# Kernel optimization log

Measured on AMD Instinct MI355X. Metric: run time of the kernel, lower is better.

Reference implementation:

```python
import jax, jax.numpy as jnp
import numpy as np

N_HEAD = 12

def setup_inputs() -> dict:
    key = jax.random.key(0)
    ks = jax.random.split(key, 5)
    B, T, C = 2, 2048, 768
    s = 0.02
    return {
        "x": jax.random.normal(ks[0], (B, T, C), jnp.float32),
        "c_attn_w": jax.random.normal(ks[1], (C, 3 * C), jnp.float32) * s,
        "c_attn_b": jax.random.normal(ks[2], (3 * C,), jnp.float32) * s,
        "c_proj_w": jax.random.normal(ks[3], (C, C), jnp.float32) * s,
        "c_proj_b": jax.random.normal(ks[4], (C,), jnp.float32) * s,
    }

def reference(x, c_attn_w, c_attn_b, c_proj_w, c_proj_b):
    B, T, C = x.shape
    H = N_HEAD
    D = C // H
    qkv = x @ c_attn_w + c_attn_b              # [B,T,3C]
    q, k, v = jnp.split(qkv, 3, axis=-1)
    # [B,T,C] -> [B,H,T,D]
    q = q.reshape(B, T, H, D).transpose(0, 2, 1, 3)
    k = k.reshape(B, T, H, D).transpose(0, 2, 1, 3)
    v = v.reshape(B, T, H, D).transpose(0, 2, 1, 3)
    att = jnp.einsum('bhqd,bhkd->bhqk', q, k) * (1.0 / np.sqrt(D))
    causal = jnp.tril(jnp.ones((T, T), bool))  # [T,T]
    att = jnp.where(causal[None, None], att, jnp.float32(-jnp.inf))
    att = jax.nn.softmax(att, axis=-1)
    y = jnp.einsum('bhqk,bhkd->bhqd', att, v)  # [B,H,T,D]
    y = y.transpose(0, 2, 1, 3).reshape(B, T, C)
    return y @ c_proj_w + c_proj_b
```

## Files before the change

### kernel.cpp

```cpp
#include <hip/hip_runtime.h>
#include <hip/hip_bf16.h>


using half4   = __attribute__((ext_vector_type(4))) _Float16;
using half8   = __attribute__((ext_vector_type(8))) _Float16;
using floatx4 = __attribute__((ext_vector_type(4))) float;

#define T_SEQ 2048
#define NHEAD 12
#define HDIM 64
#define C3 2304
#define CDIM 768
#define BT 4096
#define BH 24

static __device__ inline _Float16 f2h(float f) { return (_Float16)f; }

__global__ __launch_bounds__(256)
void prologue(const float* __restrict__ x, const float* __restrict__ wa,
              const float* __restrict__ wp, _Float16* __restrict__ xb,
              _Float16* __restrict__ wTa, _Float16* __restrict__ wTp) {
    __shared__ float tile[32][33];
    int blk = blockIdx.x, tid = threadIdx.x;
    if (blk < 2304) {
        const float* w; _Float16* wT; int K, N, bx, by;
        if (blk < 1728) { w = wa; wT = wTa; K = CDIM; N = C3; bx = blk % 72; by = blk / 72; }
        else { int b2 = blk - 1728; w = wp; wT = wTp; K = CDIM; N = CDIM; bx = b2 % 24; by = b2 / 24; }
        int tx = tid & 31, ty = tid >> 5;
        #pragma unroll
        for (int j = 0; j < 32; j += 8) {
            int k = by * 32 + ty + j, n = bx * 32 + tx;
            tile[ty + j][tx] = w[(long)k * N + n];
        }
        __syncthreads();
        #pragma unroll
        for (int j = 0; j < 32; j += 8) {
            int nO = bx * 32 + ty + j, kO = by * 32 + tx;
            wT[(long)nO * K + kO] = f2h(tile[tx][ty + j]);
        }
    } else {
        int b2 = blk - 2304;
        long e0 = (long)b2 * 4096 + tid * 16;
        floatx4 f0 = *(const floatx4*)&x[e0];
        floatx4 f1 = *(const floatx4*)&x[e0 + 4];
        floatx4 f2 = *(const floatx4*)&x[e0 + 8];
        floatx4 f3 = *(const floatx4*)&x[e0 + 12];
        half8 h0, h1;
        #pragma unroll
        for (int j = 0; j < 4; ++j) {
            h0[j] = f2h(f0[j]); h0[4 + j] = f2h(f1[j]);
            h1[j] = f2h(f2[j]); h1[4 + j] = f2h(f3[j]);
        }
        *(half8*)&xb[e0] = h0;
        *(half8*)&xb[e0 + 8] = h1;
    }
}

__global__ __launch_bounds__(256)
void gemm_qkv(const _Float16* __restrict__ A, const _Float16* __restrict__ Bt,
              const float* __restrict__ bias,
              _Float16* __restrict__ Qb, _Float16* __restrict__ Kb,
              _Float16* __restrict__ Vt) {
    __shared__ __align__(16) _Float16 As[128 * 72];
    __shared__ __align__(16) _Float16 Bs[96 * 72];
    const int K = CDIM;
    int tid = threadIdx.x;
    int m0 = blockIdx.x * 128, n0 = blockIdx.y * 96;
    int w = tid >> 6, l = tid & 63;
    int wm = (w >> 1) * 64, wn = (w & 1) * 48;
    int lr = l & 15, lq = l >> 4;

    int rs = tid >> 3, cs = (tid & 7) * 8;

    floatx4 acc[4][3] = {};

    half8 Ar[4], Br[3];
    #pragma unroll
    for (int j = 0; j < 4; ++j)
        Ar[j] = *(const half8*)&A[(long)(m0 + j * 32 + rs) * K + cs];
    #pragma unroll
    for (int j = 0; j < 3; ++j)
        Br[j] = *(const half8*)&Bt[(long)(n0 + j * 32 + rs) * K + cs];

    for (int kb = 0; kb < K; kb += 64) {
        #pragma unroll
        for (int j = 0; j < 4; ++j)
            *(half8*)&As[(j * 32 + rs) * 72 + cs] = Ar[j];
        #pragma unroll
        for (int j = 0; j < 3; ++j)
            *(half8*)&Bs[(j * 32 + rs) * 72 + cs] = Br[j];
        __syncthreads();
        if (kb + 64 < K) {
            #pragma unroll
            for (int j = 0; j < 4; ++j)
                Ar[j] = *(const half8*)&A[(long)(m0 + j * 32 + rs) * K + kb + 64 + cs];
            #pragma unroll
            for (int j = 0; j < 3; ++j)
                Br[j] = *(const half8*)&Bt[(long)(n0 + j * 32 + rs) * K + kb + 64 + cs];
        }
        #pragma unroll
        for (int kh = 0; kh < 2; ++kh) {
            half8 af[4], bf[3];
            #pragma unroll
            for (int i = 0; i < 4; ++i)
                af[i] = *(const half8*)&As[(wm + i * 16 + lr) * 72 + kh * 32 + lq * 8];
            #pragma unroll
            for (int i = 0; i < 3; ++i)
                bf[i] = *(const half8*)&Bs[(wn + i * 16 + lr) * 72 + kh * 32 + lq * 8];
            #pragma unroll
            for (int mi = 0; mi < 4; ++mi)
                #pragma unroll
                for (int ni = 0; ni < 3; ++ni)
                    acc[mi][ni] = __builtin_amdgcn_mfma_f32_16x16x32_f16(af[mi], bf[ni], acc[mi][ni], 0, 0, 0);
        }
        __syncthreads();
    }

    int region = n0 / CDIM;
    if (region < 2) {
        _Float16* O = region ? Kb : Qb;
        int nc0 = n0 - region * CDIM + wn;
        #pragma unroll
        for (int mi = 0; mi < 4; ++mi)
            #pragma unroll
            for (int ni = 0; ni < 3; ++ni) {
                int col = nc0 + ni * 16 + lr;
                float bsc = bias[region * CDIM + col];
                #pragma unroll
                for (int r = 0; r < 4; ++r) {
                    int row = m0 + wm + mi * 16 + lq * 4 + r;
                    O[(long)row * CDIM + col] = f2h(acc[mi][ni][r] + bsc);
                }
            }
    } else {
        #pragma unroll
        for (int mi = 0; mi < 4; ++mi)
            #pragma unroll
            for (int ni = 0; ni < 3; ++ni) {
                int cv = n0 - 2 * CDIM + wn + ni * 16 + lr;
                float bsc = bias[2 * CDIM + cv];
                int h = cv >> 6, d = cv & 63;
                int t0 = m0 + wm + mi * 16 + lq * 4;
                int bb = t0 >> 11, t = t0 & 2047;
                half4 hv;
                #pragma unroll
                for (int r = 0; r < 4; ++r) hv[r] = f2h(acc[mi][ni][r] + bsc);
                *(half4*)&Vt[(((long)bb * NHEAD + h) * HDIM + d) * T_SEQ + t] = hv;
            }
    }
}

__global__ __launch_bounds__(256)
void gemm_proj(const _Float16* __restrict__ A, const _Float16* __restrict__ Bt,
               const float* __restrict__ bias, float* __restrict__ Cout) {
    __shared__ __align__(16) _Float16 As[64 * 72];
    __shared__ __align__(16) _Float16 Bs[96 * 72];
    const int K = CDIM, N = CDIM;
    int tid = threadIdx.x;
    int m0 = blockIdx.x * 64, n0 = blockIdx.y * 96;
    int w = tid >> 6, l = tid & 63;
    int wm = (w >> 1) * 32, wn = (w & 1) * 48;
    int lr = l & 15, lq = l >> 4;

    int rs = tid >> 3, cs = (tid & 7) * 8;

    floatx4 acc[2][3] = {};

    half8 Ar[2], Br[3];
    #pragma unroll
    for (int j = 0; j < 2; ++j)
        Ar[j] = *(const half8*)&A[(long)(m0 + j * 32 + rs) * K + cs];
    #pragma unroll
    for (int j = 0; j < 3; ++j)
        Br[j] = *(const half8*)&Bt[(long)(n0 + j * 32 + rs) * K + cs];

    for (int kb = 0; kb < K; kb += 64) {
        #pragma unroll
        for (int j = 0; j < 2; ++j)
            *(half8*)&As[(j * 32 + rs) * 72 + cs] = Ar[j];
        #pragma unroll
        for (int j = 0; j < 3; ++j)
            *(half8*)&Bs[(j * 32 + rs) * 72 + cs] = Br[j];
        __syncthreads();
        if (kb + 64 < K) {
            #pragma unroll
            for (int j = 0; j < 2; ++j)
                Ar[j] = *(const half8*)&A[(long)(m0 + j * 32 + rs) * K + kb + 64 + cs];
            #pragma unroll
            for (int j = 0; j < 3; ++j)
                Br[j] = *(const half8*)&Bt[(long)(n0 + j * 32 + rs) * K + kb + 64 + cs];
        }
        #pragma unroll
        for (int kh = 0; kh < 2; ++kh) {
            half8 af[2], bf[3];
            #pragma unroll
            for (int i = 0; i < 2; ++i)
                af[i] = *(const half8*)&As[(wm + i * 16 + lr) * 72 + kh * 32 + lq * 8];
            #pragma unroll
            for (int i = 0; i < 3; ++i)
                bf[i] = *(const half8*)&Bs[(wn + i * 16 + lr) * 72 + kh * 32 + lq * 8];
            #pragma unroll
            for (int mi = 0; mi < 2; ++mi)
                #pragma unroll
                for (int ni = 0; ni < 3; ++ni)
                    acc[mi][ni] = __builtin_amdgcn_mfma_f32_16x16x32_f16(af[mi], bf[ni], acc[mi][ni], 0, 0, 0);
        }
        __syncthreads();
    }
    #pragma unroll
    for (int mi = 0; mi < 2; ++mi)
        #pragma unroll
        for (int ni = 0; ni < 3; ++ni) {
            int col = n0 + wn + ni * 16 + lr;
            float b = bias[col];
            #pragma unroll
            for (int r = 0; r < 4; ++r) {
                int row = m0 + wm + mi * 16 + lq * 4 + r;
                Cout[(long)row * N + col] = acc[mi][ni][r] + b;
            }
        }
}

__global__ __launch_bounds__(128)
void attn_kernel(const _Float16* __restrict__ Qb, const _Float16* __restrict__ Kb,
                 const _Float16* __restrict__ Vt, _Float16* __restrict__ y) {
    __shared__ __align__(16) _Float16 Ks[128 * 72];
    __shared__ __align__(16) _Float16 Vs[64 * 136];
    __shared__ __align__(16) _Float16 Ps[2][32 * 136];
    int tid = threadIdx.x;
    int w = tid >> 6, l = tid & 63;
    int lr = l & 15, lq = l >> 4;
    int i = blockIdx.x;
    int round = i >> 8, c = i & 255;
    int r_ = (round == 0) ? c : (round == 1 ? 767 - c : 256 + c);
    int qb = 31 - r_ / 24;
    int bh = r_ % 24;
    int b = bh / NHEAD, h = bh % NHEAD;
    int q0w = qb * 64 + w * 32;

    const _Float16* Qp = Qb + (long)b * T_SEQ * CDIM + h * HDIM;
    const _Float16* Kg = Kb + (long)b * T_SEQ * CDIM + h * HDIM;
    const _Float16* Vg = Vt + (long)bh * HDIM * T_SEQ;

    int kr = tid >> 3, kc = (tid & 7) * 8;
    int vr = tid >> 4, vc = (tid & 15) * 8;

    const float qscale = 0.125f * 1.44269504f;
    half8 aq[2][2];
    #pragma unroll
    for (int s2 = 0; s2 < 2; ++s2)
        #pragma unroll
        for (int kk = 0; kk < 2; ++kk) {
            aq[s2][kk] = *(const half8*)&Qp[(long)(q0w + s2 * 16 + lr) * CDIM + kk * 32 + lq * 8];
            #pragma unroll
            for (int j = 0; j < 8; ++j) aq[s2][kk][j] = f2h((float)aq[s2][kk][j] * qscale);
        }

    int nk = (qb + 2) >> 1;

    half8 Kr[8], Vr[8];
    #pragma unroll
    for (int j = 0; j < 8; ++j) {
        Kr[j] = *(const half8*)&Kg[(long)(j * 16 + kr) * CDIM + kc];
        Vr[j] = *(const half8*)&Vg[(long)(j * 8 + vr) * T_SEQ + vc];
    }

    float psum[2] = {0.f, 0.f};
    floatx4 acc[4][2] = {};
    int qrow0 = q0w + lr, qrow1 = q0w + 16 + lr;

    for (int kt = 0; kt < nk; ++kt) {
        int kbase = kt * 128;
        #pragma unroll
        for (int j = 0; j < 8; ++j) {
            *(half8*)&Ks[(j * 16 + kr) * 72 + kc] = Kr[j];
            *(half8*)&Vs[(j * 8 + vr) * 136 + vc] = Vr[j];
        }
        __syncthreads();
        if (kt + 1 < nk) {
            int nb = kbase + 128;
            #pragma unroll
            for (int j = 0; j < 8; ++j) {
                Kr[j] = *(const half8*)&Kg[(long)(nb + j * 16 + kr) * CDIM + kc];
                Vr[j] = *(const half8*)&Vg[(long)(j * 8 + vr) * T_SEQ + nb + vc];
            }
        }

        floatx4 sacc[8][2];
        #pragma unroll
        for (int s = 0; s < 8; ++s)
            #pragma unroll
            for (int s2 = 0; s2 < 2; ++s2) sacc[s][s2] = floatx4{0.f, 0.f, 0.f, 0.f};
        #pragma unroll
        for (int s = 0; s < 8; ++s) {
            #pragma unroll
            for (int kh = 0; kh < 2; ++kh) {
                half8 bk = *(const half8*)&Ks[(s * 16 + lr) * 72 + kh * 32 + lq * 8];
                sacc[s][0] = __builtin_amdgcn_mfma_f32_16x16x32_f16(bk, aq[0][kh], sacc[s][0], 0, 0, 0);
                sacc[s][1] = __builtin_amdgcn_mfma_f32_16x16x32_f16(bk, aq[1][kh], sacc[s][1], 0, 0, 0);
            }
        }

        if (kt == nk - 1) {
            #pragma unroll
            for (int s = 0; s < 8; ++s) {
                half4 hv0, hv1;
                #pragma unroll
                for (int r = 0; r < 4; ++r) {
                    int key = kbase + s * 16 + lq * 4 + r;
                    float p0 = (key > qrow0) ? 0.f : __builtin_amdgcn_exp2f(sacc[s][0][r]);
                    float p1 = (key > qrow1) ? 0.f : __builtin_amdgcn_exp2f(sacc[s][1][r]);
                    psum[0] += p0; psum[1] += p1;
                    hv0[r] = f2h(p0); hv1[r] = f2h(p1);
                }
                *(half4*)&Ps[w][(lr) * 136 + s * 16 + lq * 4] = hv0;
                *(half4*)&Ps[w][(16 + lr) * 136 + s * 16 + lq * 4] = hv1;
            }
        } else {
            #pragma unroll
            for (int s = 0; s < 8; ++s) {
                half4 hv0, hv1;
                #pragma unroll
                for (int r = 0; r < 4; ++r) {
                    float p0 = __builtin_amdgcn_exp2f(sacc[s][0][r]);
                    float p1 = __builtin_amdgcn_exp2f(sacc[s][1][r]);
                    psum[0] += p0; psum[1] += p1;
                    hv0[r] = f2h(p0); hv1[r] = f2h(p1);
                }
                *(half4*)&Ps[w][(lr) * 136 + s * 16 + lq * 4] = hv0;
                *(half4*)&Ps[w][(16 + lr) * 136 + s * 16 + lq * 4] = hv1;
            }
        }

        half8 ap[2][4];
        #pragma unroll
        for (int s2 = 0; s2 < 2; ++s2)
            #pragma unroll
            for (int kk = 0; kk < 4; ++kk)
                ap[s2][kk] = *(const half8*)&Ps[w][(s2 * 16 + lr) * 136 + kk * 32 + lq * 8];
        #pragma unroll
        for (int n = 0; n < 4; ++n) {
            #pragma unroll
            for (int kk = 0; kk < 4; ++kk) {
                half8 bv = *(const half8*)&Vs[(n * 16 + lr) * 136 + kk * 32 + lq * 8];
                acc[n][0] = __builtin_amdgcn_mfma_f32_16x16x32_f16(ap[0][kk], bv, acc[n][0], 0, 0, 0);
                acc[n][1] = __builtin_amdgcn_mfma_f32_16x16x32_f16(ap[1][kk], bv, acc[n][1], 0, 0, 0);
            }
        }
        __syncthreads();
    }

    #pragma unroll
    for (int s2 = 0; s2 < 2; ++s2) {
        float L = psum[s2];
        L += __shfl_xor(L, 16, 64);
        L += __shfl_xor(L, 32, 64);
        float Lr[4];
        #pragma unroll
        for (int r = 0; r < 4; ++r) Lr[r] = __shfl(L, lq * 4 + r, 64);
        #pragma unroll
        for (int n = 0; n < 4; ++n)
            #pragma unroll
            for (int r = 0; r < 4; ++r) {
                int row = q0w + s2 * 16 + lq * 4 + r;
                float v = acc[n][s2][r] / Lr[r];
                y[((long)(b * T_SEQ) + row) * CDIM + h * HDIM + n * 16 + lr] = f2h(v);
            }
    }
}

extern "C" void kernel_launch(void* const* d_in, const int* in_sizes, int n_in,
                              void* d_out, int out_size, void* d_ws, size_t ws_size,
                              hipStream_t stream) {
    const float* x      = (const float*)d_in[0];
    const float* w_attn = (const float*)d_in[1];
    const float* b_attn = (const float*)d_in[2];
    const float* w_proj = (const float*)d_in[3];
    const float* b_proj = (const float*)d_in[4];
    float* out = (float*)d_out;

    char* ws = (char*)d_ws;
    _Float16* xb  = (_Float16*)(ws);
    _Float16* wTa = (_Float16*)(ws + 6291456);
    _Float16* wTp = (_Float16*)(ws + 9830400);
    _Float16* Qb  = (_Float16*)(ws + 11010048);
    _Float16* Kb  = (_Float16*)(ws + 17301504);
    _Float16* Vt  = (_Float16*)(ws + 23592960);
    _Float16* yb  = (_Float16*)(ws + 29884416);

    prologue<<<3072, 256, 0, stream>>>(x, w_attn, w_proj, xb, wTa, wTp);

    gemm_qkv<<<dim3(BT / 128, C3 / 96), 256, 0, stream>>>(xb, wTa, b_attn, Qb, Kb, Vt);

    attn_kernel<<<BH * (T_SEQ / 64), 128, 0, stream>>>(Qb, Kb, Vt, yb);

    gemm_proj<<<dim3(BT / 64, CDIM / 96), 256, 0, stream>>>(yb, wTp, b_proj, out);
}
```

Before: 141.8 us.

## Fuse x fp16 conversion into QKV GEMM and split attention keys across four waves

The QKV GEMM now loads the fp32 input directly and converts it to fp16 while staging into shared memory, so the prologue no longer converts x and the xb buffer is no longer written and then read back. The attention kernel moves from 128 to 256 threads: each 64-query block is handled by four waves, two of which take the first half of every 128-key tile and two the second half, and their partial outputs and row sums are combined through shared memory at the end. This gives each block more waves and smaller per-wave register tiles to hide latency. The cost is an extra LDS reduction and barrier, plus twice as many fp32 bytes read for the GEMM A operand, which each N-tile block fetches again.

```diff
diff --git a/kernel.cpp b/kernel.cpp
--- a/kernel.cpp
+++ b/kernel.cpp
@@ -17,47 +17,29 @@
 static __device__ inline _Float16 f2h(float f) { return (_Float16)f; }
 
 __global__ __launch_bounds__(256)
-void prologue(const float* __restrict__ x, const float* __restrict__ wa,
-              const float* __restrict__ wp, _Float16* __restrict__ xb,
+void prologue(const float* __restrict__ wa, const float* __restrict__ wp,
               _Float16* __restrict__ wTa, _Float16* __restrict__ wTp) {
     __shared__ float tile[32][33];
     int blk = blockIdx.x, tid = threadIdx.x;
-    if (blk < 2304) {
-        const float* w; _Float16* wT; int K, N, bx, by;
-        if (blk < 1728) { w = wa; wT = wTa; K = CDIM; N = C3; bx = blk % 72; by = blk / 72; }
-        else { int b2 = blk - 1728; w = wp; wT = wTp; K = CDIM; N = CDIM; bx = b2 % 24; by = b2 / 24; }
-        int tx = tid & 31, ty = tid >> 5;
-        #pragma unroll
-        for (int j = 0; j < 32; j += 8) {
-            int k = by * 32 + ty + j, n = bx * 32 + tx;
-            tile[ty + j][tx] = w[(long)k * N + n];
-        }
-        __syncthreads();
-        #pragma unroll
-        for (int j = 0; j < 32; j += 8) {
-            int nO = bx * 32 + ty + j, kO = by * 32 + tx;
-            wT[(long)nO * K + kO] = f2h(tile[tx][ty + j]);
-        }
-    } else {
-        int b2 = blk - 2304;
-        long e0 = (long)b2 * 4096 + tid * 16;
-        floatx4 f0 = *(const floatx4*)&x[e0];
-        floatx4 f1 = *(const floatx4*)&x[e0 + 4];
-        floatx4 f2 = *(const floatx4*)&x[e0 + 8];
-        floatx4 f3 = *(const floatx4*)&x[e0 + 12];
-        half8 h0, h1;
-        #pragma unroll
-        for (int j = 0; j < 4; ++j) {
-            h0[j] = f2h(f0[j]); h0[4 + j] = f2h(f1[j]);
-            h1[j] = f2h(f2[j]); h1[4 + j] = f2h(f3[j]);
-        }
-        *(half8*)&xb[e0] = h0;
-        *(half8*)&xb[e0 + 8] = h1;
+    const float* w; _Float16* wT; int K, N, bx, by;
+    if (blk < 1728) { w = wa; wT = wTa; K = CDIM; N = C3; bx = blk % 72; by = blk / 72; }
+    else { int b2 = blk - 1728; w = wp; wT = wTp; K = CDIM; N = CDIM; bx = b2 % 24; by = b2 / 24; }
+    int tx = tid & 31, ty = tid >> 5;
+    #pragma unroll
+    for (int j = 0; j < 32; j += 8) {
+        int k = by * 32 + ty + j, n = bx * 32 + tx;
+        tile[ty + j][tx] = w[(long)k * N + n];
+    }
+    __syncthreads();
+    #pragma unroll
+    for (int j = 0; j < 32; j += 8) {
+        int nO = bx * 32 + ty + j, kO = by * 32 + tx;
+        wT[(long)nO * K + kO] = f2h(tile[tx][ty + j]);
     }
 }
 
 __global__ __launch_bounds__(256)
-void gemm_qkv(const _Float16* __restrict__ A, const _Float16* __restrict__ Bt,
+void gemm_qkv(const float* __restrict__ X, const _Float16* __restrict__ Bt,
               const float* __restrict__ bias,
               _Float16* __restrict__ Qb, _Float16* __restrict__ Kb,
               _Float16* __restrict__ Vt) {
@@ -74,26 +56,34 @@
 
     floatx4 acc[4][3] = {};
 
-    half8 Ar[4], Br[3];
-    #pragma unroll
-    for (int j = 0; j < 4; ++j)
-        Ar[j] = *(const half8*)&A[(long)(m0 + j * 32 + rs) * K + cs];
+    floatx4 Arf[4][2]; half8 Br[3];
+    #pragma unroll
+    for (int j = 0; j < 4; ++j) {
+        Arf[j][0] = *(const floatx4*)&X[(long)(m0 + j * 32 + rs) * K + cs];
+        Arf[j][1] = *(const floatx4*)&X[(long)(m0 + j * 32 + rs) * K + cs + 4];
+    }
     #pragma unroll
     for (int j = 0; j < 3; ++j)
         Br[j] = *(const half8*)&Bt[(long)(n0 + j * 32 + rs) * K + cs];
 
     for (int kb = 0; kb < K; kb += 64) {
         #pragma unroll
-        for (int j = 0; j < 4; ++j)
-            *(half8*)&As[(j * 32 + rs) * 72 + cs] = Ar[j];
+        for (int j = 0; j < 4; ++j) {
+            half8 h;
+            #pragma unroll
+            for (int e = 0; e < 4; ++e) { h[e] = f2h(Arf[j][0][e]); h[4 + e] = f2h(Arf[j][1][e]); }
+            *(half8*)&As[(j * 32 + rs) * 72 + cs] = h;
+        }
         #pragma unroll
         for (int j = 0; j < 3; ++j)
             *(half8*)&Bs[(j * 32 + rs) * 72 + cs] = Br[j];
         __syncthreads();
         if (kb + 64 < K) {
             #pragma unroll
-            for (int j = 0; j < 4; ++j)
-                Ar[j] = *(const half8*)&A[(long)(m0 + j * 32 + rs) * K + kb + 64 + cs];
+            for (int j = 0; j < 4; ++j) {
+                Arf[j][0] = *(const floatx4*)&X[(long)(m0 + j * 32 + rs) * K + kb + 64 + cs];
+                Arf[j][1] = *(const floatx4*)&X[(long)(m0 + j * 32 + rs) * K + kb + 64 + cs + 4];
+            }
             #pragma unroll
             for (int j = 0; j < 3; ++j)
                 Br[j] = *(const half8*)&Bt[(long)(n0 + j * 32 + rs) * K + kb + 64 + cs];
@@ -221,22 +211,23 @@
         }
 }
 
-__global__ __launch_bounds__(128)
+__global__ __launch_bounds__(256)
 void attn_kernel(const _Float16* __restrict__ Qb, const _Float16* __restrict__ Kb,
                  const _Float16* __restrict__ Vt, _Float16* __restrict__ y) {
     __shared__ __align__(16) _Float16 Ks[128 * 72];
     __shared__ __align__(16) _Float16 Vs[64 * 136];
-    __shared__ __align__(16) _Float16 Ps[2][32 * 136];
+    __shared__ __align__(16) _Float16 Ps[64 * 136];
     int tid = threadIdx.x;
     int w = tid >> 6, l = tid & 63;
     int lr = l & 15, lq = l >> 4;
+    int qs = (w & 1) * 32;
+    int kh2 = (w >> 1) * 64;
     int i = blockIdx.x;
     int round = i >> 8, c = i & 255;
     int r_ = (round == 0) ? c : (round == 1 ? 767 - c : 256 + c);
     int qb = 31 - r_ / 24;
     int bh = r_ % 24;
     int b = bh / NHEAD, h = bh % NHEAD;
-    int q0w = qb * 64 + w * 32;
 
     const _Float16* Qp = Qb + (long)b * T_SEQ * CDIM + h * HDIM;
     const _Float16* Kg = Kb + (long)b * T_SEQ * CDIM + h * HDIM;
@@ -248,77 +239,77 @@
     const float qscale = 0.125f * 1.44269504f;
     half8 aq[2][2];
     #pragma unroll
-    for (int s2 = 0; s2 < 2; ++s2)
+    for (int st = 0; st < 2; ++st)
         #pragma unroll
         for (int kk = 0; kk < 2; ++kk) {
-            aq[s2][kk] = *(const half8*)&Qp[(long)(q0w + s2 * 16 + lr) * CDIM + kk * 32 + lq * 8];
-            #pragma unroll
-            for (int j = 0; j < 8; ++j) aq[s2][kk][j] = f2h((float)aq[s2][kk][j] * qscale);
+            aq[st][kk] = *(const half8*)&Qp[(long)(qb * 64 + qs + st * 16 + lr) * CDIM + kk * 32 + lq * 8];
+            #pragma unroll
+            for (int j = 0; j < 8; ++j) aq[st][kk][j] = f2h((float)aq[st][kk][j] * qscale);
         }
 
     int nk = (qb + 2) >> 1;
 
-    half8 Kr[8], Vr[8];
-    #pragma unroll
-    for (int j = 0; j < 8; ++j) {
-        Kr[j] = *(const half8*)&Kg[(long)(j * 16 + kr) * CDIM + kc];
-        Vr[j] = *(const half8*)&Vg[(long)(j * 8 + vr) * T_SEQ + vc];
+    half8 Kr[4], Vr[4];
+    #pragma unroll
+    for (int j = 0; j < 4; ++j) {
+        Kr[j] = *(const half8*)&Kg[(long)(j * 32 + kr) * CDIM + kc];
+        Vr[j] = *(const half8*)&Vg[(long)(j * 16 + vr) * T_SEQ + vc];
     }
 
     float psum[2] = {0.f, 0.f};
     floatx4 acc[4][2] = {};
-    int qrow0 = q0w + lr, qrow1 = q0w + 16 + lr;
+    int qrow0 = qb * 64 + qs + lr, qrow1 = qb * 64 + qs + 16 + lr;
 
     for (int kt = 0; kt < nk; ++kt) {
         int kbase = kt * 128;
         #pragma unroll
-        for (int j = 0; j < 8; ++j) {
-            *(half8*)&Ks[(j * 16 + kr) * 72 + kc] = Kr[j];
-            *(half8*)&Vs[(j * 8 + vr) * 136 + vc] = Vr[j];
+        for (int j = 0; j < 4; ++j) {
+            *(half8*)&Ks[(j * 32 + kr) * 72 + kc] = Kr[j];
+            *(half8*)&Vs[(j * 16 + vr) * 136 + vc] = Vr[j];
         }
         __syncthreads();
         if (kt + 1 < nk) {
             int nb = kbase + 128;
             #pragma unroll
-            for (int j = 0; j < 8; ++j) {
-                Kr[j] = *(const half8*)&Kg[(long)(nb + j * 16 + kr) * CDIM + kc];
-                Vr[j] = *(const half8*)&Vg[(long)(j * 8 + vr) * T_SEQ + nb + vc];
-            }
-        }
-
-        floatx4 sacc[8][2];
-        #pragma unroll
-        for (int s = 0; s < 8; ++s)
-            #pragma unroll
-            for (int s2 = 0; s2 < 2; ++s2) sacc[s][s2] = floatx4{0.f, 0.f, 0.f, 0.f};
-        #pragma unroll
-        for (int s = 0; s < 8; ++s) {
-            #pragma unroll
-            for (int kh = 0; kh < 2; ++kh) {
-                half8 bk = *(const half8*)&Ks[(s * 16 + lr) * 72 + kh * 32 + lq * 8];
-                sacc[s][0] = __builtin_amdgcn_mfma_f32_16x16x32_f16(bk, aq[0][kh], sacc[s][0], 0, 0, 0);
-                sacc[s][1] = __builtin_amdgcn_mfma_f32_16x16x32_f16(bk, aq[1][kh], sacc[s][1], 0, 0, 0);
+            for (int j = 0; j < 4; ++j) {
+                Kr[j] = *(const half8*)&Kg[(long)(nb + j * 32 + kr) * CDIM + kc];
+                Vr[j] = *(const half8*)&Vg[(long)(j * 16 + vr) * T_SEQ + nb + vc];
+            }
+        }
+
+        floatx4 sacc[4][2];
+        #pragma unroll
+        for (int s = 0; s < 4; ++s)
+            #pragma unroll
+            for (int st = 0; st < 2; ++st) sacc[s][st] = floatx4{0.f, 0.f, 0.f, 0.f};
+        #pragma unroll
+        for (int s = 0; s < 4; ++s) {
+            #pragma unroll
+            for (int kk = 0; kk < 2; ++kk) {
+                half8 bk = *(const half8*)&Ks[(kh2 + s * 16 + lr) * 72 + kk * 32 + lq * 8];
+                sacc[s][0] = __builtin_amdgcn_mfma_f32_16x16x32_f16(bk, aq[0][kk], sacc[s][0], 0, 0, 0);
+                sacc[s][1] = __builtin_amdgcn_mfma_f32_16x16x32_f16(bk, aq[1][kk], sacc[s][1], 0, 0, 0);
             }
         }
 
         if (kt == nk - 1) {
             #pragma unroll
-            for (int s = 0; s < 8; ++s) {
+            for (int s = 0; s < 4; ++s) {
                 half4 hv0, hv1;
                 #pragma unroll
                 for (int r = 0; r < 4; ++r) {
-                    int key = kbase + s * 16 + lq * 4 + r;
+                    int key = kbase + kh2 + s * 16 + lq * 4 + r;
                     float p0 = (key > qrow0) ? 0.f : __builtin_amdgcn_exp2f(sacc[s][0][r]);
                     float p1 = (key > qrow1) ? 0.f : __builtin_amdgcn_exp2f(sacc[s][1][r]);
                     psum[0] += p0; psum[1] += p1;
                     hv0[r] = f2h(p0); hv1[r] = f2h(p1);
                 }
-                *(half4*)&Ps[w][(lr) * 136 + s * 16 + lq * 4] = hv0;
-                *(half4*)&Ps[w][(16 + lr) * 136 + s * 16 + lq * 4] = hv1;
+                *(half4*)&Ps[(qs + lr) * 136 + kh2 + s * 16 + lq * 4] = hv0;
+                *(half4*)&Ps[(qs + 16 + lr) * 136 + kh2 + s * 16 + lq * 4] = hv1;
             }
         } else {
             #pragma unroll
-            for (int s = 0; s < 8; ++s) {
+            for (int s = 0; s < 4; ++s) {
                 half4 hv0, hv1;
                 #pragma unroll
                 for (int r = 0; r < 4; ++r) {
@@ -327,22 +318,22 @@
                     psum[0] += p0; psum[1] += p1;
                     hv0[r] = f2h(p0); hv1[r] = f2h(p1);
                 }
-                *(half4*)&Ps[w][(lr) * 136 + s * 16 + lq * 4] = hv0;
-                *(half4*)&Ps[w][(16 + lr) * 136 + s * 16 + lq * 4] = hv1;
-            }
-        }
-
-        half8 ap[2][4];
-        #pragma unroll
-        for (int s2 = 0; s2 < 2; ++s2)
-            #pragma unroll
-            for (int kk = 0; kk < 4; ++kk)
-                ap[s2][kk] = *(const half8*)&Ps[w][(s2 * 16 + lr) * 136 + kk * 32 + lq * 8];
+                *(half4*)&Ps[(qs + lr) * 136 + kh2 + s * 16 + lq * 4] = hv0;
+                *(half4*)&Ps[(qs + 16 + lr) * 136 + kh2 + s * 16 + lq * 4] = hv1;
+            }
+        }
+
+        half8 ap[2][2];
+        #pragma unroll
+        for (int st = 0; st < 2; ++st)
+            #pragma unroll
+            for (int kk = 0; kk < 2; ++kk)
+                ap[st][kk] = *(const half8*)&Ps[(qs + st * 16 + lr) * 136 + kh2 + kk * 32 + lq * 8];
         #pragma unroll
         for (int n = 0; n < 4; ++n) {
             #pragma unroll
-            for (int kk = 0; kk < 4; ++kk) {
-                half8 bv = *(const half8*)&Vs[(n * 16 + lr) * 136 + kk * 32 + lq * 8];
+            for (int kk = 0; kk < 2; ++kk) {
+                half8 bv = *(const half8*)&Vs[(n * 16 + lr) * 136 + kh2 + kk * 32 + lq * 8];
                 acc[n][0] = __builtin_amdgcn_mfma_f32_16x16x32_f16(ap[0][kk], bv, acc[n][0], 0, 0, 0);
                 acc[n][1] = __builtin_amdgcn_mfma_f32_16x16x32_f16(ap[1][kk], bv, acc[n][1], 0, 0, 0);
             }
@@ -350,22 +341,47 @@
         __syncthreads();
     }
 
-    #pragma unroll
-    for (int s2 = 0; s2 < 2; ++s2) {
-        float L = psum[s2];
-        L += __shfl_xor(L, 16, 64);
-        L += __shfl_xor(L, 32, 64);
-        float Lr[4];
-        #pragma unroll
-        for (int r = 0; r < 4; ++r) Lr[r] = __shfl(L, lq * 4 + r, 64);
+    float* red = (float*)Ks;
+    int slot = ((w & 1) * 64 + l) * 36;
+    if (w >= 2) {
         #pragma unroll
         for (int n = 0; n < 4; ++n)
             #pragma unroll
-            for (int r = 0; r < 4; ++r) {
-                int row = q0w + s2 * 16 + lq * 4 + r;
-                float v = acc[n][s2][r] / Lr[r];
-                y[((long)(b * T_SEQ) + row) * CDIM + h * HDIM + n * 16 + lr] = f2h(v);
-            }
+            for (int st = 0; st < 2; ++st)
+                *(floatx4*)&red[slot + (n * 2 + st) * 4] = acc[n][st];
+        red[slot + 32] = psum[0];
+        red[slot + 33] = psum[1];
+    }
+    __syncthreads();
+    if (w < 2) {
+        #pragma unroll
+        for (int n = 0; n < 4; ++n)
+            #pragma unroll
+            for (int st = 0; st < 2; ++st) {
+                floatx4 t = *(const floatx4*)&red[slot + (n * 2 + st) * 4];
+                acc[n][st][0] += t[0]; acc[n][st][1] += t[1];
+                acc[n][st][2] += t[2]; acc[n][st][3] += t[3];
+            }
+        psum[0] += red[slot + 32];
+        psum[1] += red[slot + 33];
+
+        #pragma unroll
+        for (int st = 0; st < 2; ++st) {
+            float L = psum[st];
+            L += __shfl_xor(L, 16, 64);
+            L += __shfl_xor(L, 32, 64);
+            float Lr[4];
+            #pragma unroll
+            for (int r = 0; r < 4; ++r) Lr[r] = __shfl(L, lq * 4 + r, 64);
+            #pragma unroll
+            for (int n = 0; n < 4; ++n)
+                #pragma unroll
+                for (int r = 0; r < 4; ++r) {
+                    int row = qb * 64 + qs + st * 16 + lq * 4 + r;
+                    float v = acc[n][st][r] / Lr[r];
+                    y[((long)(b * T_SEQ) + row) * CDIM + h * HDIM + n * 16 + lr] = f2h(v);
+                }
+        }
     }
 }
 
@@ -380,7 +396,6 @@
     float* out = (float*)d_out;
 
     char* ws = (char*)d_ws;
-    _Float16* xb  = (_Float16*)(ws);
     _Float16* wTa = (_Float16*)(ws + 6291456);
     _Float16* wTp = (_Float16*)(ws + 9830400);
     _Float16* Qb  = (_Float16*)(ws + 11010048);
@@ -388,11 +403,11 @@
     _Float16* Vt  = (_Float16*)(ws + 23592960);
     _Float16* yb  = (_Float16*)(ws + 29884416);
 
-    prologue<<<3072, 256, 0, stream>>>(x, w_attn, w_proj, xb, wTa, wTp);
-
-    gemm_qkv<<<dim3(BT / 128, C3 / 96), 256, 0, stream>>>(xb, wTa, b_attn, Qb, Kb, Vt);
-
-    attn_kernel<<<BH * (T_SEQ / 64), 128, 0, stream>>>(Qb, Kb, Vt, yb);
+    prologue<<<2304, 256, 0, stream>>>(w_attn, w_proj, wTa, wTp);
+
+    gemm_qkv<<<dim3(BT / 128, C3 / 96), 256, 0, stream>>>(x, wTa, b_attn, Qb, Kb, Vt);
+
+    attn_kernel<<<BH * (T_SEQ / 64), 256, 0, stream>>>(Qb, Kb, Vt, yb);
 
     gemm_proj<<<dim3(BT / 64, CDIM / 96), 256, 0, stream>>>(yb, wTp, b_proj, out);
 }
```

Result: no change. 142.6 us (+0.6%).
